# Performance work log

Hardware: AMD Instinct MI355X
Metric: run time of the kernel (lower is better)

Reference implementation:

```python
import jax, jax.numpy as jnp
import numpy as np

H = 8      # n_heads
E = 128    # d_keys (== D; required by out_projection Linear(D*n_heads, D))


def setup_inputs() -> dict:
    key = jax.random.key(0)
    ks = jax.random.split(key, 11)
    B, T, D = 64, 256, 128
    s = 0.02
    return {
        "x": jax.random.normal(ks[0], (B, T, D), dtype=jnp.float32),
        "Wq": jax.random.normal(ks[1], (D, H * E), dtype=jnp.float32) * s,
        "bq": jax.random.normal(ks[2], (H * E,), dtype=jnp.float32) * s,
        "Wk": jax.random.normal(ks[3], (D, H * E), dtype=jnp.float32) * s,
        "bk": jax.random.normal(ks[4], (H * E,), dtype=jnp.float32) * s,
        "Wv": jax.random.normal(ks[5], (D, H * E), dtype=jnp.float32) * s,
        "bv": jax.random.normal(ks[6], (H * E,), dtype=jnp.float32) * s,
        "Ws": jax.random.normal(ks[7], (T, 1), dtype=jnp.float32) * s,
        "bs": jax.random.normal(ks[8], (1,), dtype=jnp.float32) * s,
        "Wo": jax.random.normal(ks[9], (H * E, D), dtype=jnp.float32) * s,
        "bo": jax.random.normal(ks[10], (D,), dtype=jnp.float32) * s,
    }


def reference(x, Wq, bq, Wk, bk, Wv, bv, Ws, bs, Wo, bo):
    B, T, D = x.shape
    # Q/K/V projections -> [B, T, H, E]
    Q = (x @ Wq + bq).reshape(B, T, H, E)
    K = (x @ Wk + bk).reshape(B, T, H, E)
    V = (x @ Wv + bv).reshape(B, T, H, E)
    scale = 1.0 / jnp.sqrt(jnp.float32(E))
    # QK^T scores over time: [B, H, T, T] (query t, key j)
    scores = jnp.einsum('bthd,bjhd->bhtj', Q, K)
    # summary projection contracts the key axis j: T -> 1  => [B, H, T, 1]
    summary = (scale * scores) @ Ws + bs
    # softmax over the query axis t (dim=-2)
    beta = jax.nn.softmax(summary, axis=-2)[..., 0]        # [B, H, T]
    # weight V per (b, t, h) and sum over time -> [B, H, E]
    beta_cal = jnp.transpose(beta, (0, 2, 1))[..., None]   # [B, T, H, 1]
    result = jnp.sum(V * beta_cal, axis=1)                 # [B, H, E]
    out = result.reshape(B, H * E) @ Wo + bo               # [B, D]
    return out
```

## Files before the change

kernel.cpp:

```cpp
#include <hip/hip_runtime.h>
#include <hip/hip_bf16.h>


#define SCALE 0.08838834764831845f
#define MAGIC 0x13579BDFu

#define BAR() __asm__ volatile("s_waitcnt lgkmcnt(0)\n\ts_barrier" ::: "memory")

__global__ __launch_bounds__(512)
void ta_one(const float* __restrict__ x,  const float* __restrict__ Wq,
            const float* __restrict__ Wk, const float* __restrict__ bk,
            const float* __restrict__ Wv, const float* __restrict__ bv,
            const float* __restrict__ Wsv,
            const float* __restrict__ Wo, const float* __restrict__ bov,
            float* __restrict__ ws, float* __restrict__ out)
{
    __shared__ __align__(16) float pA[2056];
    __shared__ __align__(16) float pB[2056];
    __shared__ __align__(16) float wsS[256];
    __shared__ __align__(16) float xwS[128];
    __shared__ __align__(16) float kwS[256];
    __shared__ __align__(16) float wqkS[256];
    __shared__ __align__(16) float betaS[2][256];
    __shared__ __align__(16) float xbS[256];
    __shared__ __align__(16) float resS[256];
    __shared__ float smx[2][4], sms[2][4];
    __shared__ float swS;

    const int tid = threadIdx.x;
    const int b = blockIdx.x, p = blockIdx.y;
    const int w = tid >> 6, l = tid & 63;
    const float* xp0 = x + (size_t)b * 32768;

    const int q5 = tid & 31, tc = tid >> 5;
    const int q6 = tid & 63, kh = tid >> 6;
    const int c8 = tid & 7,  r8 = tid >> 3;

    float4 rx[16];
    {
        const float4* xp = (const float4*)(xp0 + (size_t)(tc * 16) * 128 + 4 * q5);
        #pragma unroll
        for (int j = 0; j < 16; ++j) rx[j] = xp[(size_t)j * 32];
    }
    float4 rwk[16];
    {
        const float4* wp = (const float4*)(Wk + (size_t)(kh * 16) * 1024 + 256 * p + 4 * q6);
        #pragma unroll
        for (int j = 0; j < 16; ++j) rwk[j] = wp[(size_t)j * 256];
    }
    const float bkv = bk[256 * p + (tid & 255)];
    const float bvv = bv[256 * p + (tid & 255)];
    if (tid < 64) *(float4*)(wsS + 4 * tid) = *(const float4*)(Wsv + 4 * tid);
    BAR();

    {
        float4 acc = {0.f, 0.f, 0.f, 0.f};
        #pragma unroll
        for (int j = 0; j < 16; ++j) {
            const float s = wsS[tc * 16 + j];
            acc.x += s * rx[j].x; acc.y += s * rx[j].y;
            acc.z += s * rx[j].z; acc.w += s * rx[j].w;
        }
        *(float4*)(pA + tc * 128 + 4 * q5) = acc;
    }
    float4 rwq[16];
    {
        #pragma unroll
        for (int rr = 0; rr < 4; ++rr) {
            const int o = r8 + 64 * rr;
            const float* base = Wq + (size_t)(o & 127) * 1024 + (2 * p + (o >> 7)) * 128;
            #pragma unroll
            for (int jj = 0; jj < 4; ++jj)
                rwq[rr * 4 + jj] = *(const float4*)(base + (jj * 8 + c8) * 4);
        }
    }
    BAR();
    if (tid < 128) {
        float v = 0.f;
        #pragma unroll
        for (int g = 0; g < 16; ++g) v += pA[g * 128 + tid];
        xwS[tid] = v;
    } else if (tid < 192) {
        float v = wsS[l] + wsS[l + 64] + wsS[l + 128] + wsS[l + 192];
        #pragma unroll
        for (int off = 32; off; off >>= 1) v += __shfl_xor(v, off, 64);
        if (l == 0) swS = v;
    }
    BAR();

    {
        float4 acc = {0.f, 0.f, 0.f, 0.f};
        #pragma unroll
        for (int j = 0; j < 16; ++j) {
            const float xv = xwS[kh * 16 + j];
            acc.x += xv * rwk[j].x; acc.y += xv * rwk[j].y;
            acc.z += xv * rwk[j].z; acc.w += xv * rwk[j].w;
        }
        *(float4*)(pB + kh * 256 + 4 * q6) = acc;
    }
    float4 rxd[16];
    {
        #pragma unroll
        for (int rr = 0; rr < 4; ++rr) {
            const int t = r8 + 64 * rr;
            const float* base = xp0 + (size_t)t * 128;
            #pragma unroll
            for (int jj = 0; jj < 4; ++jj)
                rxd[rr * 4 + jj] = *(const float4*)(base + (jj * 8 + c8) * 4);
        }
    }
    BAR();
    if (tid < 256) {
        float v = swS * bkv;
        #pragma unroll
        for (int g = 0; g < 8; ++g) v += pB[g * 256 + tid];
        kwS[tid] = v;
    }
    BAR();

    {
        #pragma unroll
        for (int rr = 0; rr < 4; ++rr) {
            const int o = r8 + 64 * rr;
            const float* kp = kwS + (o >> 7) * 128;
            float a = 0.f;
            #pragma unroll
            for (int jj = 0; jj < 4; ++jj) {
                const float4 wv = rwq[rr * 4 + jj];
                const float* kk = kp + (jj * 8 + c8) * 4;
                a += wv.x * kk[0] + wv.y * kk[1] + wv.z * kk[2] + wv.w * kk[3];
            }
            pA[c8 * 257 + o] = a;
        }
    }
    BAR();
    if (tid < 256) {
        float v = 0.f;
        #pragma unroll
        for (int g = 0; g < 8; ++g) v += pA[g * 257 + tid];
        wqkS[tid] = v * SCALE;
    }
    BAR();

    {
        #pragma unroll
        for (int rr = 0; rr < 4; ++rr) {
            const int t = r8 + 64 * rr;
            float a0 = 0.f, a1 = 0.f;
            #pragma unroll
            for (int jj = 0; jj < 4; ++jj) {
                const float4 xv = rxd[rr * 4 + jj];
                const float* q0 = wqkS + (jj * 8 + c8) * 4;
                const float* q1 = wqkS + 128 + (jj * 8 + c8) * 4;
                a0 += xv.x * q0[0] + xv.y * q0[1] + xv.z * q0[2] + xv.w * q0[3];
                a1 += xv.x * q1[0] + xv.y * q1[1] + xv.z * q1[2] + xv.w * q1[3];
            }
            pA[c8 * 257 + t] = a0;
            pB[c8 * 257 + t] = a1;
        }
    }
    float4 rxe[16];
    {
        const float4* xp = (const float4*)(xp0 + (size_t)(tc * 16) * 128 + 4 * q5);
        #pragma unroll
        for (int j = 0; j < 16; ++j) rxe[j] = xp[(size_t)j * 32];
    }
    BAR();

    {
        const int t = tid & 255, hi = tid >> 8;
        const float* pS = hi ? pB : pA;
        float v = 0.f;
        #pragma unroll
        for (int g = 0; g < 8; ++g) v += pS[g * 257 + t];
        float m = v;
        #pragma unroll
        for (int off = 32; off; off >>= 1) m = fmaxf(m, __shfl_xor(m, off, 64));
        if (l == 0) smx[hi][w & 3] = m;
        BAR();
        const float M = fmaxf(fmaxf(smx[hi][0], smx[hi][1]), fmaxf(smx[hi][2], smx[hi][3]));
        const float e = __expf(v - M);
        float ssum = e;
        #pragma unroll
        for (int off = 32; off; off >>= 1) ssum += __shfl_xor(ssum, off, 64);
        if (l == 0) sms[hi][w & 3] = ssum;
        BAR();
        const float S = sms[hi][0] + sms[hi][1] + sms[hi][2] + sms[hi][3];
        betaS[hi][t] = e / S;
    }
    BAR();

    {
        float4 a0 = {0.f,0.f,0.f,0.f}, a1 = {0.f,0.f,0.f,0.f};
        #pragma unroll
        for (int j = 0; j < 16; ++j) {
            const float b0 = betaS[0][tc * 16 + j], b1 = betaS[1][tc * 16 + j];
            a0.x += b0 * rxe[j].x; a0.y += b0 * rxe[j].y;
            a0.z += b0 * rxe[j].z; a0.w += b0 * rxe[j].w;
            a1.x += b1 * rxe[j].x; a1.y += b1 * rxe[j].y;
            a1.z += b1 * rxe[j].z; a1.w += b1 * rxe[j].w;
        }
        *(float4*)(pA + tc * 128 + 4 * q5) = a0;
        *(float4*)(pB + tc * 128 + 4 * q5) = a1;
    }
    float4 rwv[16];
    {
        const float4* wp = (const float4*)(Wv + (size_t)(kh * 16) * 1024 + 256 * p + 4 * q6);
        #pragma unroll
        for (int j = 0; j < 16; ++j) rwv[j] = wp[(size_t)j * 256];
    }
    BAR();
    if (tid < 256) {
        const int hi = tid >> 7, d = tid & 127;
        const float* pp = hi ? pB : pA;
        float v = 0.f;
        #pragma unroll
        for (int g = 0; g < 16; ++g) v += pp[g * 128 + d];
        xbS[tid] = v;
    }
    BAR();

    {
        const int hi = q6 >> 5;
        float4 acc = {0.f, 0.f, 0.f, 0.f};
        #pragma unroll
        for (int j = 0; j < 16; ++j) {
            const float xv = xbS[hi * 128 + kh * 16 + j];
            acc.x += xv * rwv[j].x; acc.y += xv * rwv[j].y;
            acc.z += xv * rwv[j].z; acc.w += xv * rwv[j].w;
        }
        *(float4*)(pB + kh * 256 + 4 * q6) = acc;
    }
    float4 rwo[16];
    {
        const float4* wp = (const float4*)(Wo + (size_t)(256 * p + tc * 16) * 128 + 4 * q5);
        #pragma unroll
        for (int j = 0; j < 16; ++j) rwo[j] = wp[(size_t)j * 32];
    }
    BAR();
    if (tid < 256) {
        float v = bvv;
        #pragma unroll
        for (int g = 0; g < 8; ++g) v += pB[g * 256 + tid];
        resS[tid] = v;
    }
    BAR();

    {
        float4 acc = {0.f, 0.f, 0.f, 0.f};
        #pragma unroll
        for (int j = 0; j < 16; ++j) {
            const float rv = resS[tc * 16 + j];
            acc.x += rv * rwo[j].x; acc.y += rv * rwo[j].y;
            acc.z += rv * rwo[j].z; acc.w += rv * rwo[j].w;
        }
        *(float4*)(pA + tc * 128 + 4 * q5) = acc;
    }
    __syncthreads();

    float* part = ws;
    unsigned* flags = (unsigned*)(ws + 32768);
    if (p < 3) {
        if (tid < 128) {
            float v = 0.f;
            #pragma unroll
            for (int g = 0; g < 16; ++g) v += pA[g * 128 + tid];
            part[(size_t)(b * 4 + p) * 128 + tid] = v;
            __threadfence();
        }
        __syncthreads();
        if (tid == 0) atomicExch(&flags[b * 4 + p], MAGIC);
    } else {
        if (tid == 0) {
            while (atomicCAS(&flags[b * 4 + 0], MAGIC, MAGIC) != MAGIC) {}
            while (atomicCAS(&flags[b * 4 + 1], MAGIC, MAGIC) != MAGIC) {}
            while (atomicCAS(&flags[b * 4 + 2], MAGIC, MAGIC) != MAGIC) {}
        }
        __syncthreads();
        if (tid < 128) {
            float v = bov[tid];
            #pragma unroll
            for (int g = 0; g < 16; ++g) v += pA[g * 128 + tid];
            v += atomicAdd(&part[(size_t)(b * 4 + 0) * 128 + tid], 0.f);
            v += atomicAdd(&part[(size_t)(b * 4 + 1) * 128 + tid], 0.f);
            v += atomicAdd(&part[(size_t)(b * 4 + 2) * 128 + tid], 0.f);
            out[(size_t)b * 128 + tid] = v;
        }
    }
}

extern "C" void kernel_launch(void* const* d_in, const int* in_sizes, int n_in,
                              void* d_out, int out_size, void* d_ws, size_t ws_size,
                              hipStream_t stream) {
    const float* x  = (const float*)d_in[0];
    const float* Wq = (const float*)d_in[1];
    const float* Wk = (const float*)d_in[3];
    const float* bk = (const float*)d_in[4];
    const float* Wv = (const float*)d_in[5];
    const float* bv = (const float*)d_in[6];
    const float* Ws = (const float*)d_in[7];
    const float* Wo = (const float*)d_in[9];
    const float* bo = (const float*)d_in[10];
    float* out = (float*)d_out;
    float* ws  = (float*)d_ws;

    ta_one<<<dim3(64, 4), dim3(512), 0, stream>>>(x, Wq, Wk, bk, Wv, bv, Ws, Wo, bo, ws, out);
}
```

Measured before the change: 94.74 us.

## Stage x tile in LDS via async global_load_lds and prefetch weights earlier

The full 128KB x slice for the batch is loaded once into shared memory with asynchronous global-to-LDS loads, replacing three separate global reloads of x into registers across stages. The Wv and Wo weight prefetches are moved one stage earlier to overlap with more computation. This adds 128KB of LDS per block, which limits occupancy to one block per CU. It also depends on a partial vmcnt wait being correct for the async copies.

```diff
diff --git a/kernel.cpp b/kernel.cpp
--- a/kernel.cpp
+++ b/kernel.cpp
@@ -1,11 +1,13 @@
 #include <hip/hip_runtime.h>
-#include <hip/hip_bf16.h>
 
 
 #define SCALE 0.08838834764831845f
 #define MAGIC 0x13579BDFu
 
 #define BAR() __asm__ volatile("s_waitcnt lgkmcnt(0)\n\ts_barrier" ::: "memory")
+
+typedef const __attribute__((address_space(1))) void gvoid_t;
+typedef __attribute__((address_space(3))) void lvoid_t;
 
 __global__ __launch_bounds__(512)
 void ta_one(const float* __restrict__ x,  const float* __restrict__ Wq,
@@ -15,6 +17,7 @@
             const float* __restrict__ Wo, const float* __restrict__ bov,
             float* __restrict__ ws, float* __restrict__ out)
 {
+    __shared__ __align__(16) float xS[32768];
     __shared__ __align__(16) float pA[2056];
     __shared__ __align__(16) float pB[2056];
     __shared__ __align__(16) float wsS[256];
@@ -36,30 +39,36 @@
     const int q6 = tid & 63, kh = tid >> 6;
     const int c8 = tid & 7,  r8 = tid >> 3;
 
-    float4 rx[16];
-    {
-        const float4* xp = (const float4*)(xp0 + (size_t)(tc * 16) * 128 + 4 * q5);
-        #pragma unroll
-        for (int j = 0; j < 16; ++j) rx[j] = xp[(size_t)j * 32];
-    }
+    if (tid < 64) *(float4*)(wsS + 4 * tid) = *(const float4*)(Wsv + 4 * tid);
+    __builtin_amdgcn_sched_barrier(0);
+    {
+        #pragma unroll
+        for (int j = 0; j < 16; ++j) {
+            const int blk = j * 8 + w;
+            __builtin_amdgcn_global_load_lds(
+                (gvoid_t*)((const char*)xp0 + blk * 1024 + l * 16),
+                (lvoid_t*)((char*)xS + blk * 1024), 16, 0, 0);
+        }
+    }
+    __builtin_amdgcn_sched_barrier(0);
     float4 rwk[16];
     {
         const float4* wp = (const float4*)(Wk + (size_t)(kh * 16) * 1024 + 256 * p + 4 * q6);
         #pragma unroll
         for (int j = 0; j < 16; ++j) rwk[j] = wp[(size_t)j * 256];
     }
-    const float bkv = bk[256 * p + (tid & 255)];
-    const float bvv = bv[256 * p + (tid & 255)];
-    if (tid < 64) *(float4*)(wsS + 4 * tid) = *(const float4*)(Wsv + 4 * tid);
-    BAR();
-
-    {
+    __builtin_amdgcn_sched_barrier(0);
+    __asm__ volatile("s_waitcnt vmcnt(16) lgkmcnt(0)\n\ts_barrier" ::: "memory");
+
+    {
+        const float* xrow = xS + (tc * 16) * 128 + 4 * q5;
         float4 acc = {0.f, 0.f, 0.f, 0.f};
         #pragma unroll
         for (int j = 0; j < 16; ++j) {
             const float s = wsS[tc * 16 + j];
-            acc.x += s * rx[j].x; acc.y += s * rx[j].y;
-            acc.z += s * rx[j].z; acc.w += s * rx[j].w;
+            const float4 xv = *(const float4*)(xrow + j * 128);
+            acc.x += s * xv.x; acc.y += s * xv.y;
+            acc.z += s * xv.z; acc.w += s * xv.w;
         }
         *(float4*)(pA + tc * 128 + 4 * q5) = acc;
     }
@@ -74,6 +83,8 @@
                 rwq[rr * 4 + jj] = *(const float4*)(base + (jj * 8 + c8) * 4);
         }
     }
+    const float bkv = bk[256 * p + (tid & 255)];
+    const float bvv = bv[256 * p + (tid & 255)];
     BAR();
     if (tid < 128) {
         float v = 0.f;
@@ -98,16 +109,11 @@
         }
         *(float4*)(pB + kh * 256 + 4 * q6) = acc;
     }
-    float4 rxd[16];
-    {
-        #pragma unroll
-        for (int rr = 0; rr < 4; ++rr) {
-            const int t = r8 + 64 * rr;
-            const float* base = xp0 + (size_t)t * 128;
-            #pragma unroll
-            for (int jj = 0; jj < 4; ++jj)
-                rxd[rr * 4 + jj] = *(const float4*)(base + (jj * 8 + c8) * 4);
-        }
+    float4 rwv[16];
+    {
+        const float4* wp = (const float4*)(Wv + (size_t)(kh * 16) * 1024 + 256 * p + 4 * q6);
+        #pragma unroll
+        for (int j = 0; j < 16; ++j) rwv[j] = wp[(size_t)j * 256];
     }
     BAR();
     if (tid < 256) {
@@ -146,10 +152,11 @@
         #pragma unroll
         for (int rr = 0; rr < 4; ++rr) {
             const int t = r8 + 64 * rr;
+            const float* xrow = xS + t * 128;
             float a0 = 0.f, a1 = 0.f;
             #pragma unroll
             for (int jj = 0; jj < 4; ++jj) {
-                const float4 xv = rxd[rr * 4 + jj];
+                const float4 xv = *(const float4*)(xrow + (jj * 8 + c8) * 4);
                 const float* q0 = wqkS + (jj * 8 + c8) * 4;
                 const float* q1 = wqkS + 128 + (jj * 8 + c8) * 4;
                 a0 += xv.x * q0[0] + xv.y * q0[1] + xv.z * q0[2] + xv.w * q0[3];
@@ -159,12 +166,6 @@
             pB[c8 * 257 + t] = a1;
         }
     }
-    float4 rxe[16];
-    {
-        const float4* xp = (const float4*)(xp0 + (size_t)(tc * 16) * 128 + 4 * q5);
-        #pragma unroll
-        for (int j = 0; j < 16; ++j) rxe[j] = xp[(size_t)j * 32];
-    }
     BAR();
 
     {
@@ -191,23 +192,25 @@
     BAR();
 
     {
+        const float* xrow = xS + (tc * 16) * 128 + 4 * q5;
         float4 a0 = {0.f,0.f,0.f,0.f}, a1 = {0.f,0.f,0.f,0.f};
         #pragma unroll
         for (int j = 0; j < 16; ++j) {
             const float b0 = betaS[0][tc * 16 + j], b1 = betaS[1][tc * 16 + j];
-            a0.x += b0 * rxe[j].x; a0.y += b0 * rxe[j].y;
-            a0.z += b0 * rxe[j].z; a0.w += b0 * rxe[j].w;
-            a1.x += b1 * rxe[j].x; a1.y += b1 * rxe[j].y;
-            a1.z += b1 * rxe[j].z; a1.w += b1 * rxe[j].w;
+            const float4 xv = *(const float4*)(xrow + j * 128);
+            a0.x += b0 * xv.x; a0.y += b0 * xv.y;
+            a0.z += b0 * xv.z; a0.w += b0 * xv.w;
+            a1.x += b1 * xv.x; a1.y += b1 * xv.y;
+            a1.z += b1 * xv.z; a1.w += b1 * xv.w;
         }
         *(float4*)(pA + tc * 128 + 4 * q5) = a0;
         *(float4*)(pB + tc * 128 + 4 * q5) = a1;
     }
-    float4 rwv[16];
-    {
-        const float4* wp = (const float4*)(Wv + (size_t)(kh * 16) * 1024 + 256 * p + 4 * q6);
-        #pragma unroll
-        for (int j = 0; j < 16; ++j) rwv[j] = wp[(size_t)j * 256];
+    float4 rwo[16];
+    {
+        const float4* wp = (const float4*)(Wo + (size_t)(256 * p + tc * 16) * 128 + 4 * q5);
+        #pragma unroll
+        for (int j = 0; j < 16; ++j) rwo[j] = wp[(size_t)j * 32];
     }
     BAR();
     if (tid < 256) {
@@ -230,12 +233,6 @@
             acc.z += xv * rwv[j].z; acc.w += xv * rwv[j].w;
         }
         *(float4*)(pB + kh * 256 + 4 * q6) = acc;
-    }
-    float4 rwo[16];
-    {
-        const float4* wp = (const float4*)(Wo + (size_t)(256 * p + tc * 16) * 128 + 4 * q5);
-        #pragma unroll
-        for (int j = 0; j < 16; ++j) rwo[j] = wp[(size_t)j * 32];
     }
     BAR();
     if (tid < 256) {
```

Result: no change. 94.66 us (-0.1%).
